# Kernel optimization log

Measured on AMD Instinct MI355X. Metric: run time of the kernel, lower is better.

The kernel has to match this reference:

```python
import jax, jax.numpy as jnp
import numpy as np

HIDDEN_SIZE = 512  # H * d = 8 * 64


def setup_inputs() -> dict:
    key = jax.random.key(0)
    kq, kk, kv = jax.random.split(key, 3)
    B, H, S, d = 2, 8, 4096, 64
    Q = jax.random.normal(kq, (B, H, S, d), dtype=jnp.float32)
    K = jax.random.normal(kk, (B, H, d, S), dtype=jnp.float32)  # pre-transposed, as the torch module expects
    V = jax.random.normal(kv, (B, H, S, d), dtype=jnp.float32)
    return {"Q": Q, "K": K, "V": V}


def reference(Q, K, V):
    B, H, S, d = Q.shape
    scale = 1.0 / np.sqrt(HIDDEN_SIZE).astype(np.float32)
    # e: [B,H,S,S] -- full score matrix, as in the original
    e = jnp.einsum('bhsd,bhdt->bhst', Q, K) * scale
    # FAITHFUL quirk: nn.Softmax(dim=1) normalizes over the HEAD axis, not keys
    a = jax.nn.softmax(e, axis=1)
    o = jnp.einsum('bhst,bhtd->bhsd', a, V)
    # torch .view(B, S, hidden): raw contiguous reshape of [B,H,S,d]
    return o.reshape(B, S, HIDDEN_SIZE)
```

## Files before the change

kernel.cpp:

```cpp
#include <hip/hip_runtime.h>
#include <hip/hip_fp16.h>

#define S_LEN 4096
#define NHEAD 8
#define HEADD 64
#define BM 32
#define BN 32
#define TSPLIT 8
#define TCHUNK (S_LEN / TSPLIT)
#define NTILE (TCHUNK / BN)
#define EAP 48
#define KPRE 0.0637588696f

#define KT_BYTES (2ull * NHEAD * S_LEN * HEADD * 2)
#define VT_OFF   KT_BYTES
#define PART_OFF (2 * KT_BYTES)
#define PART_U32 (16ull * NHEAD * 2048 * 64)
#define WS_FULL  (PART_OFF + PART_U32 * 4)

typedef __attribute__((ext_vector_type(8))) short   short8;
typedef __attribute__((ext_vector_type(4))) float   float4v;

__device__ __forceinline__ unsigned short f2bf(float f) {
  unsigned int u = __float_as_uint(f);
  u += 0x7FFFu + ((u >> 16) & 1u);
  return (unsigned short)(u >> 16);
}
__device__ __forceinline__ float fast_exp2(float x) {
  float r; asm("v_exp_f32 %0, %1" : "=v"(r) : "v"(x)); return r;
}

__global__ __launch_bounds__(256)
void prepass_cvt(const float* __restrict__ K, const float* __restrict__ V,
                 unsigned short* __restrict__ Kt, unsigned short* __restrict__ Vt) {
  __shared__ __align__(16) unsigned short lds[64][72];
  const int tid = threadIdx.x;
  const int isV = blockIdx.x >> 10;
  const int idx = blockIdx.x & 1023;
  const int bh  = idx >> 6;
  const int t0  = (idx & 63) << 6;
  if (!isV) {
    const float* in = K + (size_t)bh * HEADD * S_LEN;
#pragma unroll
    for (int j = 0; j < 16; ++j) {
      int li = j * 256 + tid;
      int k = li >> 6, t = li & 63;
      lds[t][k] = f2bf(in[(size_t)k * S_LEN + t0 + t] * KPRE);
    }
    __syncthreads();
    unsigned short* out = Kt + (size_t)bh * S_LEN * HEADD;
    int t = tid >> 2, k0 = (tid & 3) << 4;
    *(short8*)(out + (size_t)(t0 + t) * HEADD + k0)     = *(const short8*)&lds[t][k0];
    *(short8*)(out + (size_t)(t0 + t) * HEADD + k0 + 8) = *(const short8*)&lds[t][k0 + 8];
  } else {
    const float* in = V + (size_t)bh * S_LEN * HEADD;
#pragma unroll
    for (int j = 0; j < 16; ++j) {
      int li = j * 256 + tid;
      int t = li >> 6, d = li & 63;
      lds[d][t] = f2bf(in[(size_t)(t0 + t) * HEADD + d]);
    }
    __syncthreads();
    unsigned short* out = Vt + (size_t)bh * HEADD * S_LEN;
    int d = tid >> 2, c0 = (tid & 3) << 4;
    *(short8*)(out + (size_t)d * S_LEN + t0 + c0)     = *(const short8*)&lds[d][c0];
    *(short8*)(out + (size_t)d * S_LEN + t0 + c0 + 8) = *(const short8*)&lds[d][c0 + 8];
  }
}

__global__ __launch_bounds__(512, 6)
void attn_main(const float* __restrict__ Q, const unsigned short* __restrict__ Kt,
               const unsigned short* __restrict__ Vt, unsigned int* __restrict__ part) {
  __shared__ __align__(16) unsigned short EA[2][NHEAD][BM][EAP];

  const int tid  = threadIdx.x;
  const int h    = tid >> 6;
  const int lane = tid & 63;
  const int quad = lane >> 4;
  const int l15  = lane & 15;
  const int combo = blockIdx.x & 15;
  const int b  = combo & 1;
  const int tc = combo >> 1;
  const int s0 = (blockIdx.x >> 4) * BM;

  const float* Qg = Q + (size_t)(b * NHEAD + h) * S_LEN * HEADD;
  const unsigned short* Kth = Kt + (size_t)(b * NHEAD + h) * S_LEN * HEADD;
  const unsigned short* Vth = Vt + (size_t)(b * NHEAD + h) * HEADD * S_LEN;

  short8 qf[2][2];
#pragma unroll
  for (int ss = 0; ss < 2; ++ss)
#pragma unroll
    for (int kk = 0; kk < 2; ++kk) {
      const float* p = Qg + (size_t)(s0 + ss * 16 + l15) * HEADD + kk * 32 + quad * 8;
      float4v a0 = *(const float4v*)p;
      float4v a1 = *(const float4v*)(p + 4);
      short8 f;
      f[0] = (short)f2bf(a0[0]); f[1] = (short)f2bf(a0[1]);
      f[2] = (short)f2bf(a0[2]); f[3] = (short)f2bf(a0[3]);
      f[4] = (short)f2bf(a1[0]); f[5] = (short)f2bf(a1[1]);
      f[6] = (short)f2bf(a1[2]); f[7] = (short)f2bf(a1[3]);
      qf[ss][kk] = f;
    }

  float4v acc[2][4];
#pragma unroll
  for (int ss = 0; ss < 2; ++ss)
#pragma unroll
    for (int df = 0; df < 4; ++df)
      acc[ss][df] = (float4v){0.f, 0.f, 0.f, 0.f};

  const int s_sm = tid >> 4;
  const int tp   = tid & 15;

  int t0 = tc * TCHUNK;
  for (int it = 0; it < NTILE; ++it, t0 += BN) {
    const int p = it & 1;

    {
      short8 kf[2][2];
#pragma unroll
      for (int ts = 0; ts < 2; ++ts)
#pragma unroll
        for (int kh = 0; kh < 2; ++kh)
          kf[ts][kh] = *(const short8*)(Kth + (size_t)(t0 + ts * 16 + l15) * HEADD + kh * 32 + quad * 8);
#pragma unroll
      for (int ss = 0; ss < 2; ++ss)
#pragma unroll
        for (int ts = 0; ts < 2; ++ts) {
          float4v e = (float4v){0.f, 0.f, 0.f, 0.f};
          e = __builtin_amdgcn_mfma_f32_16x16x32_bf16(qf[ss][0], kf[ts][0], e, 0, 0, 0);
          e = __builtin_amdgcn_mfma_f32_16x16x32_bf16(qf[ss][1], kf[ts][1], e, 0, 0, 0);
#pragma unroll
          for (int r = 0; r < 4; ++r)
            EA[p][h][ss * 16 + quad * 4 + r][ts * 16 + l15] =
                __half_as_ushort(__float2half(e[r]));
        }
    }
    __syncthreads();

    {
      unsigned int x[8];
#pragma unroll
      for (int hh = 0; hh < 8; ++hh)
        x[hh] = *(const unsigned int*)&EA[p][hh][s_sm][tp * 2];
      {
        float pe[8]; float sum = 0.f;
#pragma unroll
        for (int hh = 0; hh < 8; ++hh) {
          pe[hh] = fast_exp2(__half2float(__ushort_as_half((unsigned short)(x[hh] & 0xffffu))));
          sum += pe[hh];
        }
        float inv = __builtin_amdgcn_rcpf(sum);
#pragma unroll
        for (int hh = 0; hh < 8; ++hh) {
          unsigned int u = __float_as_uint(pe[hh] * inv) + 0x8000u;
          EA[p][hh][s_sm][tp * 2] = (unsigned short)(u >> 16);
        }
      }
      {
        float pe[8]; float sum = 0.f;
#pragma unroll
        for (int hh = 0; hh < 8; ++hh) {
          pe[hh] = fast_exp2(__half2float(__ushort_as_half((unsigned short)(x[hh] >> 16))));
          sum += pe[hh];
        }
        float inv = __builtin_amdgcn_rcpf(sum);
#pragma unroll
        for (int hh = 0; hh < 8; ++hh) {
          unsigned int u = __float_as_uint(pe[hh] * inv) + 0x8000u;
          EA[p][hh][s_sm][tp * 2 + 1] = (unsigned short)(u >> 16);
        }
      }
    }
    __syncthreads();

    {
      short8 vf[4];
#pragma unroll
      for (int df = 0; df < 4; ++df)
        vf[df] = *(const short8*)(Vth + (size_t)(df * 16 + l15) * S_LEN + t0 + quad * 8);
      short8 af[2];
#pragma unroll
      for (int ss = 0; ss < 2; ++ss)
        af[ss] = *(const short8*)&EA[p][h][ss * 16 + l15][quad * 8];
#pragma unroll
      for (int ss = 0; ss < 2; ++ss)
#pragma unroll
        for (int df = 0; df < 4; ++df)
          acc[ss][df] = __builtin_amdgcn_mfma_f32_16x16x32_bf16(af[ss], vf[df], acc[ss][df], 0, 0, 0);
    }
  }

  unsigned int* pb = part + ((size_t)(tc * 2 + b) * NHEAD + h) * (2048ull * 64);
  const int spb = (s0 >> 1) + quad * 2;
#pragma unroll
  for (int ss = 0; ss < 2; ++ss)
#pragma unroll
    for (int df = 0; df < 4; ++df)
#pragma unroll
      for (int rp = 0; rp < 2; ++rp) {
        unsigned int ulo = __float_as_uint(acc[ss][df][rp * 2])     + 0x8000u;
        unsigned int uhi = __float_as_uint(acc[ss][df][rp * 2 + 1]) + 0x8000u;
        unsigned int pk  = __builtin_amdgcn_perm(uhi, ulo, 0x07060302u);
        pb[(size_t)(spb + ss * 8 + rp) * 64 + df * 16 + l15] = pk;
      }
}

__global__ __launch_bounds__(256)
void reduce_partials(const unsigned int* __restrict__ part, float* __restrict__ out) {
  const size_t TCSTRIDE = 2097152;
  size_t i = ((size_t)blockIdx.x * 256 + threadIdx.x) * 4;
  if (i >= TCSTRIDE) return;
  float lo[4] = {0.f, 0.f, 0.f, 0.f}, hi[4] = {0.f, 0.f, 0.f, 0.f};
#pragma unroll
  for (int tc = 0; tc < 8; ++tc) {
    uint4 v = *(const uint4*)(part + tc * TCSTRIDE + i);
    lo[0] += __uint_as_float(v.x << 16); hi[0] += __uint_as_float(v.x & 0xffff0000u);
    lo[1] += __uint_as_float(v.y << 16); hi[1] += __uint_as_float(v.y & 0xffff0000u);
    lo[2] += __uint_as_float(v.z << 16); hi[2] += __uint_as_float(v.z & 0xffff0000u);
    lo[3] += __uint_as_float(v.w << 16); hi[3] += __uint_as_float(v.w & 0xffff0000u);
  }
  size_t bh = i >> 17;
  unsigned int r = (unsigned int)(i & 131071u);
  unsigned int sp = r >> 6, d = r & 63u;
  float* o = out + ((size_t)bh * S_LEN + 2 * sp) * HEADD + d;
  *(float4v*)o        = (float4v){lo[0], lo[1], lo[2], lo[3]};
  *(float4v*)(o + 64) = (float4v){hi[0], hi[1], hi[2], hi[3]};
}

__global__ __launch_bounds__(512, 2)
void attn_fallback(const float* __restrict__ Qg0, const float* __restrict__ Kg0,
                   const float* __restrict__ Vg0, float* __restrict__ Og0) {
  __shared__ __align__(16) unsigned short Klds[NHEAD][32][72];
  __shared__ __align__(16) unsigned short Vlds[NHEAD][HEADD][40];
  __shared__ __align__(16) unsigned short EA2[NHEAD][64][40];
  const int tid = threadIdx.x, h = tid >> 6, lane = tid & 63, quad = lane >> 4, l15 = lane & 15;
  const int b = blockIdx.x >> 6, s0 = (blockIdx.x & 63) * 64;
  const float* Qg = Qg0 + ((size_t)(b * NHEAD + h)) * S_LEN * HEADD;
  const float* Kg = Kg0 + ((size_t)(b * NHEAD + h)) * HEADD * S_LEN;
  const float* Vg = Vg0 + ((size_t)(b * NHEAD + h)) * S_LEN * HEADD;
  float* Og = Og0 + ((size_t)(b * NHEAD + h)) * S_LEN * HEADD;
  const float SC = 0.04419417382415922f;
  short8 qf[4][2];
#pragma unroll
  for (int ss = 0; ss < 4; ++ss)
#pragma unroll
    for (int kk = 0; kk < 2; ++kk) {
      const float* p = Qg + (size_t)(s0 + ss * 16 + l15) * HEADD + kk * 32 + quad * 8;
      float4v a0 = *(const float4v*)p; float4v a1 = *(const float4v*)(p + 4);
      short8 f;
      f[0] = (short)f2bf(a0[0]); f[1] = (short)f2bf(a0[1]); f[2] = (short)f2bf(a0[2]); f[3] = (short)f2bf(a0[3]);
      f[4] = (short)f2bf(a1[0]); f[5] = (short)f2bf(a1[1]); f[6] = (short)f2bf(a1[2]); f[7] = (short)f2bf(a1[3]);
      qf[ss][kk] = f;
    }
  float4v acc[4][4];
#pragma unroll
  for (int ss = 0; ss < 4; ++ss)
#pragma unroll
    for (int ds = 0; ds < 4; ++ds) acc[ss][ds] = (float4v){0.f, 0.f, 0.f, 0.f};
  const int koct = lane >> 3, kt4 = (lane & 7) * 4, vdq = lane & 15, vtg = lane >> 4;
  const int s_sm = tid >> 3, t4_sm = (tid & 7) * 4;
  for (int it = 0; it < S_LEN / 32; ++it) {
    const int t0 = it * 32;
    {
      float buf[8][4];
#pragma unroll
      for (int j = 0; j < 8; ++j) {
        float4v v = *(const float4v*)(Kg + (size_t)(koct * 8 + j) * S_LEN + t0 + kt4);
        buf[j][0] = v[0]; buf[j][1] = v[1]; buf[j][2] = v[2]; buf[j][3] = v[3];
      }
#pragma unroll
      for (int c = 0; c < 4; ++c) {
        short8 f;
#pragma unroll
        for (int j = 0; j < 8; ++j) f[j] = (short)f2bf(buf[j][c]);
        *(short8*)&Klds[h][kt4 + c][koct * 8] = f;
      }
    }
    {
      float buf[8][4];
#pragma unroll
      for (int j = 0; j < 8; ++j) {
        float4v v = *(const float4v*)(Vg + (size_t)(t0 + vtg * 8 + j) * HEADD + vdq * 4);
        buf[j][0] = v[0]; buf[j][1] = v[1]; buf[j][2] = v[2]; buf[j][3] = v[3];
      }
#pragma unroll
      for (int c = 0; c < 4; ++c) {
        short8 f;
#pragma unroll
        for (int j = 0; j < 8; ++j) f[j] = (short)f2bf(buf[j][c]);
        *(short8*)&Vlds[h][vdq * 4 + c][vtg * 8] = f;
      }
    }
    __syncthreads();
#pragma unroll
    for (int ts = 0; ts < 2; ++ts) {
      short8 kf0 = *(const short8*)&Klds[h][ts * 16 + l15][quad * 8];
      short8 kf1 = *(const short8*)&Klds[h][ts * 16 + l15][32 + quad * 8];
#pragma unroll
      for (int ss = 0; ss < 4; ++ss) {
        float4v e = (float4v){0.f, 0.f, 0.f, 0.f};
        e = __builtin_amdgcn_mfma_f32_16x16x32_bf16(qf[ss][0], kf0, e, 0, 0, 0);
        e = __builtin_amdgcn_mfma_f32_16x16x32_bf16(qf[ss][1], kf1, e, 0, 0, 0);
#pragma unroll
        for (int r = 0; r < 4; ++r)
          EA2[h][ss * 16 + quad * 4 + r][ts * 16 + l15] = __half_as_ushort(__float2half(e[r] * SC));
      }
    }
    __syncthreads();
    {
      float ev[8][4];
#pragma unroll
      for (int hh = 0; hh < 8; ++hh) {
        unsigned long long u = *(const unsigned long long*)&EA2[hh][s_sm][t4_sm];
        ev[hh][0] = __half2float(__ushort_as_half((unsigned short)u));
        ev[hh][1] = __half2float(__ushort_as_half((unsigned short)(u >> 16)));
        ev[hh][2] = __half2float(__ushort_as_half((unsigned short)(u >> 32)));
        ev[hh][3] = __half2float(__ushort_as_half((unsigned short)(u >> 48)));
      }
#pragma unroll
      for (int c = 0; c < 4; ++c) {
        float m = ev[0][c];
#pragma unroll
        for (int hh = 1; hh < 8; ++hh) m = fmaxf(m, ev[hh][c]);
        float sum = 0.f;
#pragma unroll
        for (int hh = 0; hh < 8; ++hh) { float x = __expf(ev[hh][c] - m); ev[hh][c] = x; sum += x; }
        float inv = __builtin_amdgcn_rcpf(sum);
#pragma unroll
        for (int hh = 0; hh < 8; ++hh) ev[hh][c] *= inv;
      }
#pragma unroll
      for (int hh = 0; hh < 8; ++hh) {
        unsigned short u0 = f2bf(ev[hh][0]), u1 = f2bf(ev[hh][1]), u2 = f2bf(ev[hh][2]), u3 = f2bf(ev[hh][3]);
        unsigned long long w = (unsigned long long)u0 | ((unsigned long long)u1 << 16) |
                               ((unsigned long long)u2 << 32) | ((unsigned long long)u3 << 48);
        *(unsigned long long*)&EA2[hh][s_sm][t4_sm] = w;
      }
    }
    __syncthreads();
    {
      short8 af[4], vf[4];
#pragma unroll
      for (int ss = 0; ss < 4; ++ss) af[ss] = *(const short8*)&EA2[h][ss * 16 + l15][quad * 8];
#pragma unroll
      for (int ds = 0; ds < 4; ++ds) vf[ds] = *(const short8*)&Vlds[h][ds * 16 + l15][quad * 8];
#pragma unroll
      for (int ss = 0; ss < 4; ++ss)
#pragma unroll
        for (int ds = 0; ds < 4; ++ds)
          acc[ss][ds] = __builtin_amdgcn_mfma_f32_16x16x32_bf16(af[ss], vf[ds], acc[ss][ds], 0, 0, 0);
    }
    __syncthreads();
  }
#pragma unroll
  for (int ss = 0; ss < 4; ++ss)
#pragma unroll
    for (int ds = 0; ds < 4; ++ds)
#pragma unroll
      for (int r = 0; r < 4; ++r)
        Og[(size_t)(s0 + ss * 16 + quad * 4 + r) * HEADD + ds * 16 + l15] = acc[ss][ds][r];
}

extern "C" void kernel_launch(void* const* d_in, const int* in_sizes, int n_in,
                              void* d_out, int out_size, void* d_ws, size_t ws_size,
                              hipStream_t stream) {
  const float* Q = (const float*)d_in[0];
  const float* K = (const float*)d_in[1];
  const float* V = (const float*)d_in[2];
  float* O = (float*)d_out;

  if (ws_size >= WS_FULL) {
    unsigned short* Kt = (unsigned short*)d_ws;
    unsigned short* Vt = (unsigned short*)((char*)d_ws + VT_OFF);
    unsigned int* part = (unsigned int*)((char*)d_ws + PART_OFF);
    hipLaunchKernelGGL(prepass_cvt, dim3(2048), dim3(256), 0, stream, K, V, Kt, Vt);
    hipLaunchKernelGGL(attn_main, dim3(2048), dim3(512), 0, stream, Q, Kt, Vt, part);
    hipLaunchKernelGGL(reduce_partials, dim3(2048), dim3(256), 0, stream, part, O);
  } else {
    hipLaunchKernelGGL(attn_fallback, dim3(128), dim3(512), 0, stream, Q, K, V, O);
  }
}
```

Before: 361.6 us.

## Rewrite K/V conversion prepass as register transpose without LDS; shrink EA padding

The bf16 conversion prepass drops its LDS staging and barrier. Each wave now loads 8x4 float tiles with vector loads, transposes them in registers, and writes short8 rows, so the grid is halved. The EA LDS row padding drops from 48 to 40 elements, which cuts shared memory per block and may change bank-conflict behaviour. The inline v_exp_f32 is replaced with exp2f, and the block-to-combo index mapping is rewritten in a form that yields the same values. The wider strided global accesses in the prepass may coalesce less well than the old LDS path, and exp2f may add extra instructions.

```diff
diff --git a/kernel.cpp b/kernel.cpp
--- a/kernel.cpp
+++ b/kernel.cpp
@@ -1,5 +1,6 @@
 #include <hip/hip_runtime.h>
 #include <hip/hip_fp16.h>
+#include <cmath>
 
 #define S_LEN 4096
 #define NHEAD 8
@@ -9,7 +10,7 @@
 #define TSPLIT 8
 #define TCHUNK (S_LEN / TSPLIT)
 #define NTILE (TCHUNK / BN)
-#define EAP 48
+#define EAP 40
 #define KPRE 0.0637588696f
 
 #define KT_BYTES (2ull * NHEAD * S_LEN * HEADD * 2)
@@ -26,45 +27,52 @@
   u += 0x7FFFu + ((u >> 16) & 1u);
   return (unsigned short)(u >> 16);
 }
-__device__ __forceinline__ float fast_exp2(float x) {
-  float r; asm("v_exp_f32 %0, %1" : "=v"(r) : "v"(x)); return r;
-}
 
 __global__ __launch_bounds__(256)
 void prepass_cvt(const float* __restrict__ K, const float* __restrict__ V,
                  unsigned short* __restrict__ Kt, unsigned short* __restrict__ Vt) {
-  __shared__ __align__(16) unsigned short lds[64][72];
-  const int tid = threadIdx.x;
-  const int isV = blockIdx.x >> 10;
-  const int idx = blockIdx.x & 1023;
-  const int bh  = idx >> 6;
-  const int t0  = (idx & 63) << 6;
+  const int tid  = threadIdx.x;
+  const int wave = tid >> 6, lane = tid & 63;
+  const int isV  = blockIdx.x >> 9;
+  const int idx  = blockIdx.x & 511;
+  const int bh   = idx >> 5;
+  const int t0   = (idx & 31) * 128 + wave * 32;
   if (!isV) {
     const float* in = K + (size_t)bh * HEADD * S_LEN;
-#pragma unroll
-    for (int j = 0; j < 16; ++j) {
-      int li = j * 256 + tid;
-      int k = li >> 6, t = li & 63;
-      lds[t][k] = f2bf(in[(size_t)k * S_LEN + t0 + t] * KPRE);
-    }
-    __syncthreads();
     unsigned short* out = Kt + (size_t)bh * S_LEN * HEADD;
-    int t = tid >> 2, k0 = (tid & 3) << 4;
-    *(short8*)(out + (size_t)(t0 + t) * HEADD + k0)     = *(const short8*)&lds[t][k0];
-    *(short8*)(out + (size_t)(t0 + t) * HEADD + k0 + 8) = *(const short8*)&lds[t][k0 + 8];
+    const int koct = lane >> 3;
+    const int kt4  = (lane & 7) * 4;
+    float buf[8][4];
+#pragma unroll
+    for (int j = 0; j < 8; ++j) {
+      float4v v = *(const float4v*)(in + (size_t)(koct * 8 + j) * S_LEN + t0 + kt4);
+      buf[j][0] = v[0]; buf[j][1] = v[1]; buf[j][2] = v[2]; buf[j][3] = v[3];
+    }
+#pragma unroll
+    for (int c = 0; c < 4; ++c) {
+      short8 f;
+#pragma unroll
+      for (int j = 0; j < 8; ++j) f[j] = (short)f2bf(buf[j][c] * KPRE);
+      *(short8*)(out + (size_t)(t0 + kt4 + c) * HEADD + koct * 8) = f;
+    }
   } else {
     const float* in = V + (size_t)bh * S_LEN * HEADD;
-#pragma unroll
-    for (int j = 0; j < 16; ++j) {
-      int li = j * 256 + tid;
-      int t = li >> 6, d = li & 63;
-      lds[d][t] = f2bf(in[(size_t)(t0 + t) * HEADD + d]);
-    }
-    __syncthreads();
     unsigned short* out = Vt + (size_t)bh * HEADD * S_LEN;
-    int d = tid >> 2, c0 = (tid & 3) << 4;
-    *(short8*)(out + (size_t)d * S_LEN + t0 + c0)     = *(const short8*)&lds[d][c0];
-    *(short8*)(out + (size_t)d * S_LEN + t0 + c0 + 8) = *(const short8*)&lds[d][c0 + 8];
+    const int vdq = lane & 15;
+    const int vtg = lane >> 4;
+    float buf[8][4];
+#pragma unroll
+    for (int j = 0; j < 8; ++j) {
+      float4v v = *(const float4v*)(in + (size_t)(t0 + vtg * 8 + j) * HEADD + vdq * 4);
+      buf[j][0] = v[0]; buf[j][1] = v[1]; buf[j][2] = v[2]; buf[j][3] = v[3];
+    }
+#pragma unroll
+    for (int c = 0; c < 4; ++c) {
+      short8 f;
+#pragma unroll
+      for (int j = 0; j < 8; ++j) f[j] = (short)f2bf(buf[j][c]);
+      *(short8*)(out + (size_t)(vdq * 4 + c) * S_LEN + t0 + vtg * 8) = f;
+    }
   }
 }
 
@@ -78,7 +86,7 @@
   const int lane = tid & 63;
   const int quad = lane >> 4;
   const int l15  = lane & 15;
-  const int combo = blockIdx.x & 15;
+  const int combo = (blockIdx.x & 7) | (((blockIdx.x >> 3) & 1) << 3);
   const int b  = combo & 1;
   const int tc = combo >> 1;
   const int s0 = (blockIdx.x >> 4) * BM;
@@ -113,9 +121,11 @@
   const int s_sm = tid >> 4;
   const int tp   = tid & 15;
 
-  int t0 = tc * TCHUNK;
-  for (int it = 0; it < NTILE; ++it, t0 += BN) {
-    const int p = it & 1;
+  const int tbase = tc * TCHUNK;
+
+  for (int it = 0; it < NTILE; ++it) {
+    const int t0 = tbase + it * BN;
+    const int p  = it & 1;
 
     {
       short8 kf[2][2];
@@ -148,7 +158,7 @@
         float pe[8]; float sum = 0.f;
 #pragma unroll
         for (int hh = 0; hh < 8; ++hh) {
-          pe[hh] = fast_exp2(__half2float(__ushort_as_half((unsigned short)(x[hh] & 0xffffu))));
+          pe[hh] = exp2f(__half2float(__ushort_as_half((unsigned short)(x[hh] & 0xffffu))));
           sum += pe[hh];
         }
         float inv = __builtin_amdgcn_rcpf(sum);
@@ -162,7 +172,7 @@
         float pe[8]; float sum = 0.f;
 #pragma unroll
         for (int hh = 0; hh < 8; ++hh) {
-          pe[hh] = fast_exp2(__half2float(__ushort_as_half((unsigned short)(x[hh] >> 16))));
+          pe[hh] = exp2f(__half2float(__ushort_as_half((unsigned short)(x[hh] >> 16))));
           sum += pe[hh];
         }
         float inv = __builtin_amdgcn_rcpf(sum);
@@ -375,7 +385,7 @@
     unsigned short* Kt = (unsigned short*)d_ws;
     unsigned short* Vt = (unsigned short*)((char*)d_ws + VT_OFF);
     unsigned int* part = (unsigned int*)((char*)d_ws + PART_OFF);
-    hipLaunchKernelGGL(prepass_cvt, dim3(2048), dim3(256), 0, stream, K, V, Kt, Vt);
+    hipLaunchKernelGGL(prepass_cvt, dim3(1024), dim3(256), 0, stream, K, V, Kt, Vt);
     hipLaunchKernelGGL(attn_main, dim3(2048), dim3(512), 0, stream, Q, Kt, Vt, part);
     hipLaunchKernelGGL(reduce_partials, dim3(2048), dim3(256), 0, stream, part, O);
   } else {
```

Result: faster. 353.2 us (-2.3%).
